# Optimization experiments

Measured on AMD Instinct MI355X. Metric: run time of the kernel, lower is better.

## Reference

```python
import jax, jax.numpy as jnp
import numpy as np

V, E, H, A, S, B = 32000, 1024, 1024, 10, 512, 64


def setup_inputs() -> dict:
    key = jax.random.key(0)
    ks = jax.random.split(key, 12)
    s = 0.02
    return {
        "dec_input": jax.random.randint(ks[0], (B, 1), 0, V, dtype=jnp.int32),
        "dec_hidden": jax.random.normal(ks[1], (1, B, H), jnp.float32),
        "enc_outputs": jax.random.normal(ks[2], (S, B, H), jnp.float32),
        "emb": jax.random.normal(ks[3], (V, E), jnp.float32) * s,
        "Wa1": jax.random.normal(ks[4], (A, 2 * H), jnp.float32) * s,  # attention layer 1, no bias
        "Wa2": jax.random.normal(ks[5], (1, A), jnp.float32) * s,      # attention layer 2, no bias
        "W_ih": jax.random.normal(ks[6], (3 * H, E + H), jnp.float32) * s,  # GRU input weights (r,z,n)
        "W_hh": jax.random.normal(ks[7], (3 * H, H), jnp.float32) * s,      # GRU hidden weights (r,z,n)
        "b_ih": jnp.zeros((3 * H,), jnp.float32),
        "b_hh": jnp.zeros((3 * H,), jnp.float32),
        "W_out": jax.random.normal(ks[8], (V, H), jnp.float32) * s,
        "b_out": jnp.zeros((V,), jnp.float32),
    }


def reference(dec_input, dec_hidden, enc_outputs, emb, Wa1, Wa2, W_ih, W_hh, b_ih, b_hh, W_out, b_out):
    h_last = dec_hidden[-1]  # [B, H]
    # Bahdanau additive attention over encoder time steps (axis 0)
    hh = jnp.broadcast_to(h_last[None], enc_outputs.shape)        # [S, B, H]
    feats = jnp.concatenate([hh, enc_outputs], axis=-1)           # [S, B, 2H]
    e = jnp.tanh(feats @ Wa1.T) @ Wa2.T                           # [S, B, 1]
    alpha = jax.nn.softmax(e, axis=0)                             # softmax over seq
    c = jnp.sum(alpha * enc_outputs, axis=0)                      # [B, H]
    # embedding lookup for the single decoder step
    x = emb[dec_input[:, 0]]                                      # [B, E]
    xc = jnp.concatenate([x, c], axis=1)                          # [B, E+H]
    # single-step GRU (PyTorch gate order: r, z, n)
    gi = xc @ W_ih.T + b_ih                                       # [B, 3H]
    gh = h_last @ W_hh.T + b_hh                                   # [B, 3H]
    i_r, i_z, i_n = jnp.split(gi, 3, axis=1)
    h_r, h_z, h_n = jnp.split(gh, 3, axis=1)
    r = jax.nn.sigmoid(i_r + h_r)
    z = jax.nn.sigmoid(i_z + h_z)
    n = jnp.tanh(i_n + r * h_n)
    h_new = (1.0 - z) * n + z * h_last                            # [B, H]
    logits = h_new @ W_out.T + b_out                              # [B, V]
    return logits, h_new[None]                                    # ([B,V], [1,B,H])
```

## Files before the change

### kernel.cpp

```cpp
#include <hip/hip_runtime.h>
#include <math.h>

#define Vv 32000
#define Ee 1024
#define Hh 1024
#define Aa 10
#define Ss 512
#define Bb 64
#define Mm (Ss * Bb)

typedef __attribute__((ext_vector_type(8))) short bf16x8;
typedef __attribute__((ext_vector_type(4))) short s16x4;
typedef __attribute__((ext_vector_type(4))) float f32x4;

__device__ inline short f2bf(float f) {
    union { float f; unsigned int u; } v;
    v.f = f;
    unsigned int r = (v.u + 0x7FFFu + ((v.u >> 16) & 1u)) >> 16;
    return (short)r;
}

__device__ inline bf16x8 cvt8(float4 lo, float4 hi) {
    bf16x8 r;
    r[0] = f2bf(lo.x); r[1] = f2bf(lo.y); r[2] = f2bf(lo.z); r[3] = f2bf(lo.w);
    r[4] = f2bf(hi.x); r[5] = f2bf(hi.y); r[6] = f2bf(hi.z); r[7] = f2bf(hi.w);
    return r;
}

__global__ __launch_bounds__(256) void hpart_kernel(const float* __restrict__ Wa1,
                                                    const float* __restrict__ h,
                                                    float* __restrict__ hpart) {
    __shared__ float red[256];
    const int b = blockIdx.x, t = threadIdx.x;
    float p[Aa];
#pragma unroll
    for (int a = 0; a < Aa; a++) p[a] = 0.f;
    for (int k = t; k < Hh; k += 256) {
        float hv = h[b * Hh + k];
#pragma unroll
        for (int a = 0; a < Aa; a++) p[a] += Wa1[a * (2 * Hh) + k] * hv;
    }
    for (int a = 0; a < Aa; a++) {
        red[t] = p[a];
        __syncthreads();
        for (int o = 128; o > 0; o >>= 1) {
            if (t < o) red[t] += red[t + o];
            __syncthreads();
        }
        if (t == 0) hpart[b * 16 + a] = red[0];
        __syncthreads();
    }
}

__global__ __launch_bounds__(256) void scores_mfma_kernel(
    const float* __restrict__ enc,
    const float* __restrict__ Wa1,
    float* __restrict__ epre) {
    const int t = threadIdx.x;
    const int w = t >> 6, lane = t & 63;
    const int col = lane & 15, quad = lane >> 4;
    const int m0 = (blockIdx.x * 4 + w) * 16;
    const int p = blockIdx.y;
    const int kb0 = p * 512;

    f32x4 acc = {0.f, 0.f, 0.f, 0.f};
    const int wa_row = (col < Aa) ? col : 0;
    const float* wrow = Wa1 + (size_t)wa_row * (2 * Hh) + Hh + kb0 + quad * 8;
    const float* arow = enc + (size_t)(m0 + col) * Hh + kb0 + quad * 8;
    const bool valid = (col < Aa);

#pragma unroll
    for (int c = 0; c < 16; c++) {
        float4 a0 = *(const float4*)(arow + c * 32);
        float4 a1 = *(const float4*)(arow + c * 32 + 4);
        bf16x8 af = cvt8(a0, a1);
        bf16x8 bf;
        if (valid) {
            float4 b0 = *(const float4*)(wrow + c * 32);
            float4 b1 = *(const float4*)(wrow + c * 32 + 4);
            bf = cvt8(b0, b1);
        } else {
            bf = (bf16x8){0, 0, 0, 0, 0, 0, 0, 0};
        }
        acc = __builtin_amdgcn_mfma_f32_16x16x32_bf16(af, bf, acc, 0, 0, 0);
    }
    float* out = epre + ((size_t)p * Mm + m0) * 16;
#pragma unroll
    for (int r = 0; r < 4; r++)
        out[(quad * 4 + r) * 16 + col] = acc[r];
}

__global__ __launch_bounds__(512) void softmax_kernel(const float* __restrict__ epre,
                                                      const float* __restrict__ hpart,
                                                      const float* __restrict__ Wa2,
                                                      float* __restrict__ alpha) {
    __shared__ float red[512];
    const int b = blockIdx.x, s = threadIdx.x;
    const int m = s * Bb + b;
    float v = 0.f;
#pragma unroll
    for (int a = 0; a < Aa; a++) {
        float tot = hpart[b * 16 + a] + epre[(size_t)m * 16 + a]
                    + epre[((size_t)Mm + m) * 16 + a];
        v += Wa2[a] * tanhf(tot);
    }
    red[s] = v;
    __syncthreads();
    for (int o = 256; o > 0; o >>= 1) {
        if (s < o) red[s] = fmaxf(red[s], red[s + o]);
        __syncthreads();
    }
    float mx = red[0];
    __syncthreads();
    float ex = expf(v - mx);
    red[s] = ex;
    __syncthreads();
    for (int o = 256; o > 0; o >>= 1) {
        if (s < o) red[s] += red[s + o];
        __syncthreads();
    }
    float inv = 1.f / red[0];
    alpha[s * Bb + b] = ex * inv;
}

__global__ __launch_bounds__(256) void context_kernel(const float* __restrict__ enc,
                                                      const float* __restrict__ alpha,
                                                      float* __restrict__ cpart) {
    const int b = blockIdx.x, sc = blockIdx.y;
    const int h4 = threadIdx.x;
    const float4* enc4 = (const float4*)enc;
    float4 acc = {0.f, 0.f, 0.f, 0.f};
    const int s0 = sc * 32;
    for (int s = s0; s < s0 + 32; ++s) {
        float a = alpha[s * Bb + b];
        float4 ev = enc4[(size_t)(s * Bb + b) * 256 + h4];
        acc.x += a * ev.x;
        acc.y += a * ev.y;
        acc.z += a * ev.z;
        acc.w += a * ev.w;
    }
    ((float4*)cpart)[((size_t)sc * Bb + b) * 256 + h4] = acc;
}

__global__ __launch_bounds__(256) void xc_kernel(const int* __restrict__ dec_input,
                                                 const float* __restrict__ emb,
                                                 const float* __restrict__ cpart,
                                                 const float* __restrict__ h,
                                                 short* __restrict__ xcb,
                                                 short* __restrict__ hb) {
    const int b = blockIdx.x, t = threadIdx.x;
    const int tok = dec_input[b];
    float4 cv = {0.f, 0.f, 0.f, 0.f};
#pragma unroll
    for (int p = 0; p < 16; p++) {
        float4 v = ((const float4*)cpart)[((size_t)p * Bb + b) * 256 + t];
        cv.x += v.x; cv.y += v.y; cv.z += v.z; cv.w += v.w;
    }
    float4 ev = ((const float4*)(emb + (size_t)tok * Ee))[t];
    float4 hv = ((const float4*)(h + (size_t)b * Hh))[t];
    s16x4 e4 = {f2bf(ev.x), f2bf(ev.y), f2bf(ev.z), f2bf(ev.w)};
    s16x4 c4 = {f2bf(cv.x), f2bf(cv.y), f2bf(cv.z), f2bf(cv.w)};
    s16x4 h4v = {f2bf(hv.x), f2bf(hv.y), f2bf(hv.z), f2bf(hv.w)};
    ((s16x4*)(xcb + (size_t)b * 2048))[t] = e4;
    ((s16x4*)(xcb + (size_t)b * 2048 + 1024))[t] = c4;
    ((s16x4*)(hb + (size_t)b * 1024))[t] = h4v;
}

__global__ __launch_bounds__(256) void gemm_mfma_kernel(
    const short* __restrict__ Abf,
    const float* __restrict__ W,
    const float* __restrict__ bias,
    float* __restrict__ C,
    int N, int K, int Klen) {
    const int t = threadIdx.x;
    const int w = t >> 6, lane = t & 63;
    const int col = lane & 15, quad = lane >> 4;
    const int n0 = blockIdx.x * 64 + w * 16;
    const int kb0 = blockIdx.y * Klen;

    f32x4 acc[4];
#pragma unroll
    for (int mt = 0; mt < 4; mt++) acc[mt] = (f32x4){0.f, 0.f, 0.f, 0.f};

    const float* wrow = W + (size_t)(n0 + col) * K + kb0 + quad * 8;
    const short* arow = Abf + (size_t)col * K + kb0 + quad * 8;

    for (int kb = 0; kb < Klen; kb += 64) {
        float4 w0 = *(const float4*)(wrow + kb);
        float4 w1 = *(const float4*)(wrow + kb + 4);
        float4 w2 = *(const float4*)(wrow + kb + 32);
        float4 w3 = *(const float4*)(wrow + kb + 36);
        bf16x8 bf0 = cvt8(w0, w1);
        bf16x8 bf1 = cvt8(w2, w3);
        bf16x8 a0[4], a1[4];
#pragma unroll
        for (int mt = 0; mt < 4; mt++) {
            a0[mt] = *(const bf16x8*)(arow + (size_t)mt * 16 * K + kb);
            a1[mt] = *(const bf16x8*)(arow + (size_t)mt * 16 * K + kb + 32);
        }
#pragma unroll
        for (int mt = 0; mt < 4; mt++)
            acc[mt] = __builtin_amdgcn_mfma_f32_16x16x32_bf16(a0[mt], bf0, acc[mt], 0, 0, 0);
#pragma unroll
        for (int mt = 0; mt < 4; mt++)
            acc[mt] = __builtin_amdgcn_mfma_f32_16x16x32_bf16(a1[mt], bf1, acc[mt], 0, 0, 0);
    }

    const float bv = (bias != nullptr) ? bias[n0 + col] : 0.f;
    float* Cp = C + (size_t)blockIdx.y * 64 * N;
#pragma unroll
    for (int mt = 0; mt < 4; mt++) {
#pragma unroll
        for (int r = 0; r < 4; r++) {
            int m = mt * 16 + quad * 4 + r;
            Cp[(size_t)m * N + n0 + col] = acc[mt][r] + bv;
        }
    }
}

__global__ __launch_bounds__(256) void gru_kernel(const float* __restrict__ gip,
                                                  const float* __restrict__ ghp,
                                                  const float* __restrict__ b_ih,
                                                  const float* __restrict__ b_hh,
                                                  const float* __restrict__ h,
                                                  float* __restrict__ h_new,
                                                  short* __restrict__ hnb) {
    const int idx = blockIdx.x * 256 + threadIdx.x;
    const int b = idx >> 10, j = idx & 1023;
    const size_t base = (size_t)b * (3 * Hh);
    float ir = b_ih[j], iz = b_ih[Hh + j], in_ = b_ih[2 * Hh + j];
    float hr = b_hh[j], hz = b_hh[Hh + j], hn = b_hh[2 * Hh + j];
#pragma unroll
    for (int p = 0; p < 8; p++) {
        const float* g = gip + (size_t)p * Bb * 3 * Hh + base;
        ir += g[j]; iz += g[Hh + j]; in_ += g[2 * Hh + j];
    }
#pragma unroll
    for (int p = 0; p < 8; p++) {
        const float* g = ghp + (size_t)p * Bb * 3 * Hh + base;
        hr += g[j]; hz += g[Hh + j]; hn += g[2 * Hh + j];
    }
    float r = 1.f / (1.f + expf(-(ir + hr)));
    float z = 1.f / (1.f + expf(-(iz + hz)));
    float n = tanhf(in_ + r * hn);
    float val = (1.f - z) * n + z * h[idx];
    h_new[idx] = val;
    hnb[idx] = f2bf(val);
}

extern "C" void kernel_launch(void* const* d_in, const int* in_sizes, int n_in,
                              void* d_out, int out_size, void* d_ws, size_t ws_size,
                              hipStream_t stream) {
    const int* dec_input = (const int*)d_in[0];
    const float* dec_hidden = (const float*)d_in[1];
    const float* enc = (const float*)d_in[2];
    const float* emb = (const float*)d_in[3];
    const float* Wa1 = (const float*)d_in[4];
    const float* Wa2 = (const float*)d_in[5];
    const float* W_ih = (const float*)d_in[6];
    const float* W_hh = (const float*)d_in[7];
    const float* b_ih = (const float*)d_in[8];
    const float* b_hh = (const float*)d_in[9];
    const float* W_out = (const float*)d_in[10];
    const float* b_out = (const float*)d_in[11];

    float* out = (float*)d_out;
    float* logits = out;
    float* h_new = out + (size_t)Bb * Vv;

    float* ws = (float*)d_ws;
    float* alpha_ptr = ws;
    float* hpart_ptr = ws + 32768;
    short* xcb_ptr = (short*)(ws + 33792);
    short* hb_ptr = (short*)(ws + 99328);
    short* hnb_ptr = (short*)(ws + 132096);
    float* region1 = ws + 164864;
    float* region2 = ws + 1737728;
    float* epre_ptr = region1;
    float* gip_ptr = region1;
    float* cpart_ptr = region2;
    float* ghp_ptr = region2;

    hpart_kernel<<<Bb, 256, 0, stream>>>(Wa1, dec_hidden, hpart_ptr);
    scores_mfma_kernel<<<dim3(Mm / 64, 2), 256, 0, stream>>>(enc, Wa1, epre_ptr);
    softmax_kernel<<<Bb, 512, 0, stream>>>(epre_ptr, hpart_ptr, Wa2, alpha_ptr);
    context_kernel<<<dim3(Bb, 16), 256, 0, stream>>>(enc, alpha_ptr, cpart_ptr);
    xc_kernel<<<Bb, 256, 0, stream>>>(dec_input, emb, cpart_ptr, dec_hidden,
                                      xcb_ptr, hb_ptr);

    gemm_mfma_kernel<<<dim3(3 * Hh / 64, 8), 256, 0, stream>>>(
        xcb_ptr, W_ih, nullptr, gip_ptr, 3 * Hh, Ee + Hh, 256);
    gemm_mfma_kernel<<<dim3(3 * Hh / 64, 8), 256, 0, stream>>>(
        hb_ptr, W_hh, nullptr, ghp_ptr, 3 * Hh, Hh, 128);

    gru_kernel<<<(Bb * Hh) / 256, 256, 0, stream>>>(gip_ptr, ghp_ptr, b_ih, b_hh,
                                                    dec_hidden, h_new, hnb_ptr);

    gemm_mfma_kernel<<<dim3(Vv / 64, 1), 256, 0, stream>>>(
        hnb_ptr, W_out, b_out, logits, Vv, Hh, 1024);
}
```

Before: 448.3 us.

## Fuse attention tanh/Wa2 epilogue into scores MFMA and softmax into context kernel

The scores kernel now covers the full K=1024 range in one pass instead of two K-halves, and applies hpart, tanh and the Wa2 projection in its epilogue, writing per-(b,s) energies in a transposed layout. The separate softmax kernel is removed; each context block recomputes the max/sum normalization over 512 energies using wave shuffles before accumulating. The hpart reduction also uses shuffles instead of a shared-memory tree, and the GEMM K/Klen become template parameters with partial unrolling. This cuts one launch and the large epre intermediate. The costs are half as many scores blocks, and each context block (16 per batch row) redundantly repeating the softmax.

```diff
diff --git a/kernel.cpp b/kernel.cpp
--- a/kernel.cpp
+++ b/kernel.cpp
@@ -30,49 +30,58 @@
 __global__ __launch_bounds__(256) void hpart_kernel(const float* __restrict__ Wa1,
                                                     const float* __restrict__ h,
                                                     float* __restrict__ hpart) {
-    __shared__ float red[256];
+    __shared__ float part[4][16];
     const int b = blockIdx.x, t = threadIdx.x;
+    const int w = t >> 6, lane = t & 63;
+    const float* hb_ = h + (size_t)b * Hh;
     float p[Aa];
 #pragma unroll
     for (int a = 0; a < Aa; a++) p[a] = 0.f;
-    for (int k = t; k < Hh; k += 256) {
-        float hv = h[b * Hh + k];
+#pragma unroll
+    for (int i = 0; i < 4; i++) {
+        const int k = w * 256 + i * 64 + lane;
+        const float hv = hb_[k];
 #pragma unroll
         for (int a = 0; a < Aa; a++) p[a] += Wa1[a * (2 * Hh) + k] * hv;
     }
+#pragma unroll
     for (int a = 0; a < Aa; a++) {
-        red[t] = p[a];
-        __syncthreads();
-        for (int o = 128; o > 0; o >>= 1) {
-            if (t < o) red[t] += red[t + o];
-            __syncthreads();
-        }
-        if (t == 0) hpart[b * 16 + a] = red[0];
-        __syncthreads();
-    }
-}
-
-__global__ __launch_bounds__(256) void scores_mfma_kernel(
+        float v = p[a];
+        v += __shfl_xor(v, 1, 64);
+        v += __shfl_xor(v, 2, 64);
+        v += __shfl_xor(v, 4, 64);
+        v += __shfl_xor(v, 8, 64);
+        v += __shfl_xor(v, 16, 64);
+        v += __shfl_xor(v, 32, 64);
+        if (lane == 0) part[w][a] = v;
+    }
+    __syncthreads();
+    if (t < Aa)
+        hpart[b * 16 + t] = part[0][t] + part[1][t] + part[2][t] + part[3][t];
+}
+
+__global__ __launch_bounds__(256) void scores_e_kernel(
     const float* __restrict__ enc,
     const float* __restrict__ Wa1,
-    float* __restrict__ epre) {
+    const float* __restrict__ Wa2,
+    const float* __restrict__ hpart,
+    float* __restrict__ e_t) {
     const int t = threadIdx.x;
     const int w = t >> 6, lane = t & 63;
     const int col = lane & 15, quad = lane >> 4;
     const int m0 = (blockIdx.x * 4 + w) * 16;
-    const int p = blockIdx.y;
-    const int kb0 = p * 512;
+    const int bb = m0 & 63;
+    const bool valid = (col < Aa);
+    const int wa_row = valid ? col : 0;
+
+    const float* erow = enc + (size_t)(m0 + col) * Hh + quad * 8;
+    const float* wrow = Wa1 + (size_t)wa_row * (2 * Hh) + Hh + quad * 8;
 
     f32x4 acc = {0.f, 0.f, 0.f, 0.f};
-    const int wa_row = (col < Aa) ? col : 0;
-    const float* wrow = Wa1 + (size_t)wa_row * (2 * Hh) + Hh + kb0 + quad * 8;
-    const float* arow = enc + (size_t)(m0 + col) * Hh + kb0 + quad * 8;
-    const bool valid = (col < Aa);
-
-#pragma unroll
-    for (int c = 0; c < 16; c++) {
-        float4 a0 = *(const float4*)(arow + c * 32);
-        float4 a1 = *(const float4*)(arow + c * 32 + 4);
+#pragma unroll 4
+    for (int c = 0; c < 32; c++) {
+        float4 a0 = *(const float4*)(erow + c * 32);
+        float4 a1 = *(const float4*)(erow + c * 32 + 4);
         bf16x8 af = cvt8(a0, a1);
         bf16x8 bf;
         if (valid) {
@@ -84,62 +93,79 @@
         }
         acc = __builtin_amdgcn_mfma_f32_16x16x32_bf16(af, bf, acc, 0, 0, 0);
     }
-    float* out = epre + ((size_t)p * Mm + m0) * 16;
-#pragma unroll
-    for (int r = 0; r < 4; r++)
-        out[(quad * 4 + r) * 16 + col] = acc[r];
-}
-
-__global__ __launch_bounds__(512) void softmax_kernel(const float* __restrict__ epre,
-                                                      const float* __restrict__ hpart,
-                                                      const float* __restrict__ Wa2,
-                                                      float* __restrict__ alpha) {
-    __shared__ float red[512];
-    const int b = blockIdx.x, s = threadIdx.x;
-    const int m = s * Bb + b;
-    float v = 0.f;
-#pragma unroll
-    for (int a = 0; a < Aa; a++) {
-        float tot = hpart[b * 16 + a] + epre[(size_t)m * 16 + a]
-                    + epre[((size_t)Mm + m) * 16 + a];
-        v += Wa2[a] * tanhf(tot);
-    }
-    red[s] = v;
+
+    const float w2 = valid ? Wa2[col] : 0.f;
+    float v[4];
+#pragma unroll
+    for (int r = 0; r < 4; r++) {
+        const int mr = quad * 4 + r;
+        const float hp = valid ? hpart[(bb + mr) * 16 + col] : 0.f;
+        v[r] = w2 * tanhf(acc[r] + hp);
+    }
+#pragma unroll
+    for (int r = 0; r < 4; r++) {
+        v[r] += __shfl_xor(v[r], 1, 16);
+        v[r] += __shfl_xor(v[r], 2, 16);
+        v[r] += __shfl_xor(v[r], 4, 16);
+        v[r] += __shfl_xor(v[r], 8, 16);
+    }
+    if (col == 0) {
+#pragma unroll
+        for (int r = 0; r < 4; r++) {
+            const int m = m0 + quad * 4 + r;
+            e_t[(size_t)(m & 63) * Ss + (m >> 6)] = v[r];
+        }
+    }
+}
+
+__global__ __launch_bounds__(256) void context_kernel(const float* __restrict__ enc,
+                                                      const float* __restrict__ e_t,
+                                                      float* __restrict__ cpart) {
+    __shared__ float al[Ss];
+    __shared__ float sred[8];
+    const int b = blockIdx.x, sc = blockIdx.y, t = threadIdx.x;
+    const int w = t >> 6, lane = t & 63;
+
+    const float x0 = e_t[(size_t)b * Ss + t];
+    const float x1 = e_t[(size_t)b * Ss + 256 + t];
+    float mx = fmaxf(x0, x1);
+    mx = fmaxf(mx, __shfl_xor(mx, 1, 64));
+    mx = fmaxf(mx, __shfl_xor(mx, 2, 64));
+    mx = fmaxf(mx, __shfl_xor(mx, 4, 64));
+    mx = fmaxf(mx, __shfl_xor(mx, 8, 64));
+    mx = fmaxf(mx, __shfl_xor(mx, 16, 64));
+    mx = fmaxf(mx, __shfl_xor(mx, 32, 64));
+    if (lane == 0) sred[w] = mx;
     __syncthreads();
-    for (int o = 256; o > 0; o >>= 1) {
-        if (s < o) red[s] = fmaxf(red[s], red[s + o]);
-        __syncthreads();
-    }
-    float mx = red[0];
+    const float MX = fmaxf(fmaxf(sred[0], sred[1]), fmaxf(sred[2], sred[3]));
+    const float e0 = expf(x0 - MX), e1 = expf(x1 - MX);
+    al[t] = e0;
+    al[t + 256] = e1;
+    float su = e0 + e1;
+    su += __shfl_xor(su, 1, 64);
+    su += __shfl_xor(su, 2, 64);
+    su += __shfl_xor(su, 4, 64);
+    su += __shfl_xor(su, 8, 64);
+    su += __shfl_xor(su, 16, 64);
+    su += __shfl_xor(su, 32, 64);
+    if (lane == 0) sred[4 + w] = su;
     __syncthreads();
-    float ex = expf(v - mx);
-    red[s] = ex;
-    __syncthreads();
-    for (int o = 256; o > 0; o >>= 1) {
-        if (s < o) red[s] += red[s + o];
-        __syncthreads();
-    }
-    float inv = 1.f / red[0];
-    alpha[s * Bb + b] = ex * inv;
-}
-
-__global__ __launch_bounds__(256) void context_kernel(const float* __restrict__ enc,
-                                                      const float* __restrict__ alpha,
-                                                      float* __restrict__ cpart) {
-    const int b = blockIdx.x, sc = blockIdx.y;
-    const int h4 = threadIdx.x;
+    const float inv = 1.f / (sred[4] + sred[5] + sred[6] + sred[7]);
+
     const float4* enc4 = (const float4*)enc;
     float4 acc = {0.f, 0.f, 0.f, 0.f};
     const int s0 = sc * 32;
-    for (int s = s0; s < s0 + 32; ++s) {
-        float a = alpha[s * Bb + b];
-        float4 ev = enc4[(size_t)(s * Bb + b) * 256 + h4];
+#pragma unroll 4
+    for (int i = 0; i < 32; ++i) {
+        const int s = s0 + i;
+        const float a = al[s] * inv;
+        float4 ev = enc4[(size_t)(s * Bb + b) * 256 + t];
         acc.x += a * ev.x;
         acc.y += a * ev.y;
         acc.z += a * ev.z;
         acc.w += a * ev.w;
     }
-    ((float4*)cpart)[((size_t)sc * Bb + b) * 256 + h4] = acc;
+    ((float4*)cpart)[((size_t)sc * Bb + b) * 256 + t] = acc;
 }
 
 __global__ __launch_bounds__(256) void xc_kernel(const int* __restrict__ dec_input,
@@ -166,17 +192,18 @@
     ((s16x4*)(hb + (size_t)b * 1024))[t] = h4v;
 }
 
+template<int K, int KLEN>
 __global__ __launch_bounds__(256) void gemm_mfma_kernel(
     const short* __restrict__ Abf,
     const float* __restrict__ W,
     const float* __restrict__ bias,
     float* __restrict__ C,
-    int N, int K, int Klen) {
+    int N) {
     const int t = threadIdx.x;
     const int w = t >> 6, lane = t & 63;
     const int col = lane & 15, quad = lane >> 4;
     const int n0 = blockIdx.x * 64 + w * 16;
-    const int kb0 = blockIdx.y * Klen;
+    const int kb0 = blockIdx.y * KLEN;
 
     f32x4 acc[4];
 #pragma unroll
@@ -185,7 +212,8 @@
     const float* wrow = W + (size_t)(n0 + col) * K + kb0 + quad * 8;
     const short* arow = Abf + (size_t)col * K + kb0 + quad * 8;
 
-    for (int kb = 0; kb < Klen; kb += 64) {
+#pragma unroll 2
+    for (int kb = 0; kb < KLEN; kb += 64) {
         float4 w0 = *(const float4*)(wrow + kb);
         float4 w1 = *(const float4*)(wrow + kb + 4);
         float4 w2 = *(const float4*)(wrow + kb + 32);
@@ -269,33 +297,31 @@
     float* h_new = out + (size_t)Bb * Vv;
 
     float* ws = (float*)d_ws;
-    float* alpha_ptr = ws;
-    float* hpart_ptr = ws + 32768;
+    float* hpart_ptr = ws;
+    float* e_ptr = ws + 1024;
     short* xcb_ptr = (short*)(ws + 33792);
     short* hb_ptr = (short*)(ws + 99328);
     short* hnb_ptr = (short*)(ws + 132096);
     float* region1 = ws + 164864;
     float* region2 = ws + 1737728;
-    float* epre_ptr = region1;
+    float* cpart_ptr = region1;
     float* gip_ptr = region1;
-    float* cpart_ptr = region2;
     float* ghp_ptr = region2;
 
     hpart_kernel<<<Bb, 256, 0, stream>>>(Wa1, dec_hidden, hpart_ptr);
-    scores_mfma_kernel<<<dim3(Mm / 64, 2), 256, 0, stream>>>(enc, Wa1, epre_ptr);
-    softmax_kernel<<<Bb, 512, 0, stream>>>(epre_ptr, hpart_ptr, Wa2, alpha_ptr);
-    context_kernel<<<dim3(Bb, 16), 256, 0, stream>>>(enc, alpha_ptr, cpart_ptr);
+    scores_e_kernel<<<Mm / 64, 256, 0, stream>>>(enc, Wa1, Wa2, hpart_ptr, e_ptr);
+    context_kernel<<<dim3(Bb, 16), 256, 0, stream>>>(enc, e_ptr, cpart_ptr);
     xc_kernel<<<Bb, 256, 0, stream>>>(dec_input, emb, cpart_ptr, dec_hidden,
                                       xcb_ptr, hb_ptr);
 
-    gemm_mfma_kernel<<<dim3(3 * Hh / 64, 8), 256, 0, stream>>>(
-        xcb_ptr, W_ih, nullptr, gip_ptr, 3 * Hh, Ee + Hh, 256);
-    gemm_mfma_kernel<<<dim3(3 * Hh / 64, 8), 256, 0, stream>>>(
-        hb_ptr, W_hh, nullptr, ghp_ptr, 3 * Hh, Hh, 128);
+    gemm_mfma_kernel<2048, 256><<<dim3(3 * Hh / 64, 8), 256, 0, stream>>>(
+        xcb_ptr, W_ih, nullptr, gip_ptr, 3 * Hh);
+    gemm_mfma_kernel<1024, 128><<<dim3(3 * Hh / 64, 8), 256, 0, stream>>>(
+        hb_ptr, W_hh, nullptr, ghp_ptr, 3 * Hh);
 
     gru_kernel<<<(Bb * Hh) / 256, 256, 0, stream>>>(gip_ptr, ghp_ptr, b_ih, b_hh,
                                                     dec_hidden, h_new, hnb_ptr);
 
-    gemm_mfma_kernel<<<dim3(Vv / 64, 1), 256, 0, stream>>>(
-        hnb_ptr, W_out, b_out, logits, Vv, Hh, 1024);
-}
+    gemm_mfma_kernel<1024, 1024><<<dim3(Vv / 64, 1), 256, 0, stream>>>(
+        hnb_ptr, W_out, b_out, logits, Vv);
+}
```

After: 447.2 us. No clear change (-0.2%).
